# Kernel optimization log

Hardware: AMD Instinct MI355X
Metric: run time of the kernel (lower is better)

The kernel has to match this reference:

```python
import jax, jax.numpy as jnp
import numpy as np

B, S, H, NH = 8, 2048, 256, 4
D = H // NH
EPS = 1e-12


def setup_inputs() -> dict:
    key = jax.random.key(0)
    ks = jax.random.split(key, 8)
    w = lambda k: jax.random.normal(k, (H, H), jnp.float32) * 0.02
    return {
        "input_tensor": jax.random.normal(ks[0], (B, S, H), jnp.float32),
        "attribute_table": jax.random.normal(ks[1], (B, S, 1, H), jnp.float32),
        "position_embedding": jax.random.normal(ks[2], (B, S, H), jnp.float32),
        "attention_mask": jnp.zeros((B, 1, S, S), jnp.float32),
        "Wq": w(ks[3]), "bq": jnp.zeros((H,), jnp.float32),
        "Wk": w(ks[4]), "bk": jnp.zeros((H,), jnp.float32),
        "Wv": w(ks[5]), "bv": jnp.zeros((H,), jnp.float32),
        "Wd": w(ks[6]), "bd": jnp.zeros((H,), jnp.float32),
        "gamma": jnp.ones((H,), jnp.float32),
        "beta": jnp.zeros((H,), jnp.float32),
    }


def _layer_norm(x, g, b):
    mu = jnp.mean(x, axis=-1, keepdims=True)
    var = jnp.mean(jnp.square(x - mu), axis=-1, keepdims=True)
    return (x - mu) * jax.lax.rsqrt(var + EPS) * g + b


def reference(input_tensor, attribute_table, position_embedding, attention_mask,
              Wq, bq, Wk, bk, Wv, bv, Wd, bd, gamma, beta):
    # fusion_type == 'sum': sum attribute tables + item emb + position emb
    mixed = jnp.sum(attribute_table, axis=-2) + input_tensor + position_embedding  # [B,S,H]
    q = (mixed @ Wq + bq).reshape(B, S, NH, D)
    k = (mixed @ Wk + bk).reshape(B, S, NH, D)
    v = (input_tensor @ Wv + bv).reshape(B, S, NH, D)  # value from raw item emb
    scores = jnp.einsum('bqhd,bkhd->bhqk', q, k) / jnp.sqrt(jnp.float32(D))
    scores = scores + attention_mask  # additive mask broadcast over heads
    probs = jax.nn.softmax(scores, axis=-1)  # attn_dropout p=0 (eval)
    ctx = jnp.einsum('bhqk,bkhd->bqhd', probs, v).reshape(B, S, H)
    hidden = ctx @ Wd + bd  # out_dropout p=0 (eval)
    return _layer_norm(hidden + input_tensor, gamma, beta)
```

## Files before the change

kernel.cpp:

```cpp
#include <hip/hip_runtime.h>
#include <hip/hip_bf16.h>
#include <math.h>

#define BB 8
#define SS 2048
#define HH 256
#define NHH 4
#define DD 64
#define MROWS (BB*SS)
#define LOG2E 1.44269504f

typedef unsigned short u16;
typedef unsigned int   u32;
typedef __attribute__((ext_vector_type(8))) short bf16x8;
typedef __attribute__((ext_vector_type(4))) float f32x4;
typedef __attribute__((ext_vector_type(8))) u16   u16x8;
typedef __attribute__((ext_vector_type(4))) u16   u16x4;

__device__ inline u16 f2bf(float f) {
    union { float f; u32 u; } v; v.f = f;
    u32 r = v.u + 0x7fffu + ((v.u >> 16) & 1u);
    return (u16)(r >> 16);
}
__device__ inline u16 f2bf_n(float f) {
    __hip_bfloat16 h = __float2bfloat16(f);
    return *(u16*)&h;
}
__device__ inline float bf2f(u16 h) {
    union { u32 u; float f; } v; v.u = (u32)h << 16; return v.f;
}
__device__ inline float fexp2(float x) {
#if __has_builtin(__builtin_amdgcn_exp2f)
    return __builtin_amdgcn_exp2f(x);
#else
    return __expf(x * 0.6931471806f);
#endif
}
__device__ inline void gload16(const u16* g, u16* l) {
    __builtin_amdgcn_global_load_lds(
        (const __attribute__((address_space(1))) u32*)g,
        (__attribute__((address_space(3))) u32*)l, 16, 0, 0);
}

__global__ __launch_bounds__(256) void fuse_mixed_cast(const float* __restrict__ inp,
    const float* __restrict__ attr, const float* __restrict__ pos,
    u16* __restrict__ mixed, u16* __restrict__ inpb, int n8) {
    int i = blockIdx.x * 256 + threadIdx.x;
    if (i >= n8) return;
    const f32x4* pi = (const f32x4*)(inp  + (size_t)i*8);
    const f32x4* pa = (const f32x4*)(attr + (size_t)i*8);
    const f32x4* pp = (const f32x4*)(pos  + (size_t)i*8);
    u16x8 om, oi;
    #pragma unroll
    for (int h = 0; h < 2; ++h) {
        f32x4 a = pi[h], b = pa[h], c = pp[h];
        #pragma unroll
        for (int j = 0; j < 4; ++j) {
            om[h*4+j] = f2bf(a[j] + b[j] + c[j]);
            oi[h*4+j] = f2bf(a[j]);
        }
    }
    *(u16x8*)(mixed + (size_t)i*8) = om;
    *(u16x8*)(inpb  + (size_t)i*8) = oi;
}

__global__ __launch_bounds__(256) void transpose_w(const float* __restrict__ W0,
    const float* __restrict__ W1, const float* __restrict__ W2,
    const float* __restrict__ W3, u16* __restrict__ Wt) {
    const float* W = blockIdx.y==0 ? W0 : blockIdx.y==1 ? W1 : blockIdx.y==2 ? W2 : W3;
    u16* dst = Wt + (size_t)blockIdx.y*65536;
    int kt = blockIdx.x & 3, nt = blockIdx.x >> 2;
    __shared__ float T[64][65];
    int tid = threadIdx.x;
    int r = tid >> 2, cq = tid & 3;
    const float* src = W + (size_t)(kt*64 + r)*HH + nt*64 + cq*16;
    #pragma unroll
    for (int j = 0; j < 4; ++j) {
        f32x4 v = ((const f32x4*)src)[j];
        T[r][cq*16 + j*4 + 0] = v[0];
        T[r][cq*16 + j*4 + 1] = v[1];
        T[r][cq*16 + j*4 + 2] = v[2];
        T[r][cq*16 + j*4 + 3] = v[3];
    }
    __syncthreads();
    u16x8 o0, o1;
    #pragma unroll
    for (int j = 0; j < 8; ++j) o0[j] = f2bf(T[cq*16 + j][r]);
    #pragma unroll
    for (int j = 0; j < 8; ++j) o1[j] = f2bf(T[cq*16 + 8 + j][r]);
    u16* d = dst + (size_t)(nt*64 + r)*HH + kt*64 + cq*16;
    *(u16x8*)d       = o0;
    *(u16x8*)(d + 8) = o1;
}

template<bool VT>
__global__ __launch_bounds__(256) void gemm_mfma(
    const u16* __restrict__ A0, const u16* __restrict__ A1,
    const u16* __restrict__ Wt, const float* __restrict__ bias0,
    const float* __restrict__ bias1, u16* __restrict__ O0, u16* __restrict__ O1)
{
    __shared__ u16 As[2][128*64];
    __shared__ u16 Ws[2][128*64];
    int tid = threadIdx.x;
    int w = tid >> 6, l = tid & 63;
    int lq = l & 15, g4 = l >> 4;
    int w0 = w >> 1, w1 = w & 1;
    int z = blockIdx.z;
    const u16* A = z ? A1 : A0;
    const u16* Wz = Wt + (size_t)z*65536;
    const float* bias = z ? bias1 : bias0;
    u16* Oz = z ? O1 : O0;
    int bm = blockIdx.x*128, bn = blockIdx.y*128;

    int rr0 = l >> 3;
    int cc0 = (l & 7) ^ (rr0 & 7);
    const u16* agp[4]; const u16* wgp[4];
    #pragma unroll
    for (int q = 0; q < 4; ++q) {
        int rr = (w*4+q)*8 + rr0;
        agp[q] = A  + (size_t)(bm + rr)*HH + cc0*8;
        wgp[q] = Wz + (size_t)(bn + rr)*HH + cc0*8;
    }

    f32x4 acc[4][4];
    #pragma unroll
    for (int i = 0; i < 4; ++i)
        #pragma unroll
        for (int j = 0; j < 4; ++j) acc[i][j] = (f32x4){0.f,0.f,0.f,0.f};

    #define STAGE(buf, k0) { \
        _Pragma("unroll") \
        for (int q = 0; q < 4; ++q) { \
            gload16(agp[q] + (k0), &As[buf][(w*4+q)*512]); \
            gload16(wgp[q] + (k0), &Ws[buf][(w*4+q)*512]); \
        } }

    STAGE(0, 0);
    __syncthreads();
    int cur = 0;
    #pragma unroll
    for (int t = 0; t < 4; ++t) {
        if (t < 3) STAGE(cur^1, (t+1)*64);
        #pragma unroll
        for (int kk = 0; kk < 2; ++kk) {
            bf16x8 af[4], wf[4];
            #pragma unroll
            for (int i = 0; i < 4; ++i) {
                int row = w0*64 + i*16 + lq;
                int cc = (kk*4 + g4) ^ (row & 7);
                af[i] = *(const bf16x8*)&As[cur][row*64 + cc*8];
            }
            #pragma unroll
            for (int j = 0; j < 4; ++j) {
                int row = w1*64 + j*16 + lq;
                int cc = (kk*4 + g4) ^ (row & 7);
                wf[j] = *(const bf16x8*)&Ws[cur][row*64 + cc*8];
            }
            #pragma unroll
            for (int i = 0; i < 4; ++i)
                #pragma unroll
                for (int j = 0; j < 4; ++j) {
                    if (VT)
                        acc[i][j] = __builtin_amdgcn_mfma_f32_16x16x32_bf16(af[i], wf[j], acc[i][j], 0,0,0);
                    else
                        acc[i][j] = __builtin_amdgcn_mfma_f32_16x16x32_bf16(wf[j], af[i], acc[i][j], 0,0,0);
                }
        }
        __syncthreads();
        cur ^= 1;
    }

    if (!VT) {
        #pragma unroll
        for (int i = 0; i < 4; ++i) {
            size_t m = bm + w0*64 + i*16 + lq;
            #pragma unroll
            for (int j = 0; j < 4; ++j) {
                int n = bn + w1*64 + j*16 + g4*4;
                f32x4 bb = *(const f32x4*)&bias[n];
                u16x4 o;
                #pragma unroll
                for (int r = 0; r < 4; ++r) o[r] = f2bf(acc[i][j][r] + bb[r]);
                *(u16x4*)&Oz[m*HH + n] = o;
            }
        }
    } else {
        int b = bm >> 11;
        int sb = bm & 2047;
        #pragma unroll
        for (int i = 0; i < 4; ++i) {
            int s = sb + w0*64 + i*16 + g4*4;
            #pragma unroll
            for (int j = 0; j < 4; ++j) {
                int n = bn + w1*64 + j*16 + lq;
                float bs = bias[n];
                int h = n >> 6, d = n & 63;
                u16x4 o;
                #pragma unroll
                for (int r = 0; r < 4; ++r) o[r] = f2bf(acc[i][j][r] + bs);
                *(u16x4*)&Oz[(((size_t)b*NHH + h)*DD + d)*SS + s] = o;
            }
        }
    }
    #undef STAGE
}

__global__ __launch_bounds__(256) void attn_mfma(
    const u16* __restrict__ Qb, const u16* __restrict__ Kb,
    const u16* __restrict__ Vt, const float* __restrict__ mask,
    u16* __restrict__ O)
{
    __shared__ u16 KT[2][64*64];
    __shared__ u16 VTs[2][64*64];
    __shared__ u16 PT[4][16*64];

    int tid = threadIdx.x;
    int w = tid >> 6, l = tid & 63;
    int lq = l & 15, g = l >> 4;
    int qb = blockIdx.x, h = blockIdx.y, b = blockIdx.z;
    int q = qb*64 + w*16 + lq;

    bf16x8 qf[2];
    {
        const u16* qp = Qb + ((size_t)(b*SS + q))*HH + h*DD + g*8;
        qf[0] = *(const bf16x8*)qp;
        qf[1] = *(const bf16x8*)(qp + 32);
    }

    int srow = tid >> 3;
    int sch  = tid & 7;
    const u16* kgp0 = Kb + ((size_t)(b*SS + srow))*HH + h*DD + sch*8;
    const u16* kgp1 = kgp0 + (size_t)32*HH;
    const u16* vgp0 = Vt + (((size_t)(b*NHH + h))*DD + srow)*SS + sch*8;
    const u16* vgp1 = vgp0 + (size_t)32*SS;
    int sidx0 = srow*64 + ((sch ^ (srow & 7)))*8;
    int sidx1 = sidx0 + 32*64;

    const float* mrow = mask + ((size_t)b*SS + q)*SS + g*4;

    f32x4 ot[4];
    #pragma unroll
    for (int dt = 0; dt < 4; ++dt) ot[dt] = (f32x4){0.f,0.f,0.f,0.f};
    float m = -1e30f, lsum = 0.f;

    u16x8 kr0 = *(const u16x8*)kgp0;
    u16x8 kr1 = *(const u16x8*)kgp1;
    u16x8 vr0 = *(const u16x8*)vgp0;
    u16x8 vr1 = *(const u16x8*)vgp1;
    f32x4 mr[2][4];
    #pragma unroll
    for (int kt = 0; kt < 4; ++kt) mr[0][kt] = *(const f32x4*)(mrow + kt*16);
    *(u16x8*)&KT[0][sidx0]  = kr0;
    *(u16x8*)&KT[0][sidx1]  = kr1;
    *(u16x8*)&VTs[0][sidx0] = vr0;
    *(u16x8*)&VTs[0][sidx1] = vr1;
    __syncthreads();

    #pragma unroll 2
    for (int t = 0; t < SS/64; ++t) {
        int cur = t & 1;
        if (t < SS/64 - 1) {
            kr0 = *(const u16x8*)(kgp0 + (size_t)(t+1)*64*HH);
            kr1 = *(const u16x8*)(kgp1 + (size_t)(t+1)*64*HH);
            vr0 = *(const u16x8*)(vgp0 + (t+1)*64);
            vr1 = *(const u16x8*)(vgp1 + (t+1)*64);
            #pragma unroll
            for (int kt = 0; kt < 4; ++kt)
                mr[cur^1][kt] = *(const f32x4*)(mrow + (t+1)*64 + kt*16);
        }

        f32x4 st[4];
        __builtin_amdgcn_s_setprio(1);
        #pragma unroll
        for (int kt = 0; kt < 4; ++kt) {
            st[kt] = (f32x4){0.f,0.f,0.f,0.f};
            int key = kt*16 + lq;
            #pragma unroll
            for (int df = 0; df < 2; ++df) {
                int c = (4*df + g) ^ (key & 7);
                bf16x8 a = *(const bf16x8*)&KT[cur][key*64 + c*8];
                st[kt] = __builtin_amdgcn_mfma_f32_16x16x32_bf16(a, qf[df], st[kt], 0,0,0);
            }
        }
        __builtin_amdgcn_s_setprio(0);

        float s[4][4];
        #pragma unroll
        for (int kt = 0; kt < 4; ++kt)
            #pragma unroll
            for (int j = 0; j < 4; ++j)
                s[kt][j] = __builtin_fmaf(st[kt][j], 0.125f, mr[cur][kt][j]);

        float cm[4];
        #pragma unroll
        for (int kt = 0; kt < 4; ++kt)
            cm[kt] = fmaxf(fmaxf(s[kt][0], s[kt][1]), fmaxf(s[kt][2], s[kt][3]));
        float tm = fmaxf(fmaxf(cm[0], cm[1]), fmaxf(cm[2], cm[3]));
        tm = fmaxf(tm, __shfl_xor(tm, 16));
        tm = fmaxf(tm, __shfl_xor(tm, 32));

        if (!__all(tm <= m + 8.0f)) {
            float mn = fmaxf(m, tm);
            float sc = fexp2((m - mn) * LOG2E);
            lsum *= sc;
            #pragma unroll
            for (int dt = 0; dt < 4; ++dt) {
                ot[dt][0] *= sc; ot[dt][1] *= sc;
                ot[dt][2] *= sc; ot[dt][3] *= sc;
            }
            m = mn;
        }
        float mnl = m * LOG2E;

        float e[4][4];
        #pragma unroll
        for (int kt = 0; kt < 4; ++kt)
            #pragma unroll
            for (int j = 0; j < 4; ++j)
                e[kt][j] = fexp2(__builtin_fmaf(s[kt][j], LOG2E, -mnl));
        float cs[4];
        #pragma unroll
        for (int kt = 0; kt < 4; ++kt)
            cs[kt] = (e[kt][0] + e[kt][1]) + (e[kt][2] + e[kt][3]);
        float rs = (cs[0] + cs[1]) + (cs[2] + cs[3]);
        rs += __shfl_xor(rs, 16);
        rs += __shfl_xor(rs, 32);
        lsum += rs;

        #pragma unroll
        for (int kt = 0; kt < 4; ++kt) {
            u16x4 pk;
            #pragma unroll
            for (int j = 0; j < 4; ++j) pk[j] = f2bf_n(e[kt][j]);
            int koff = kt*16 + g*4;
            int c = (koff >> 3) ^ (lq & 7);
            int idx = lq*64 + c*8 + (koff & 7);
            *(u16x4*)&PT[w][idx] = pk;
        }

        bf16x8 pb[2];
        #pragma unroll
        for (int kt2 = 0; kt2 < 2; ++kt2) {
            int c = (4*kt2 + g) ^ (lq & 7);
            pb[kt2] = *(const bf16x8*)&PT[w][lq*64 + c*8];
        }
        __builtin_amdgcn_s_setprio(1);
        #pragma unroll
        for (int dt = 0; dt < 4; ++dt) {
            int d = dt*16 + lq;
            #pragma unroll
            for (int kt2 = 0; kt2 < 2; ++kt2) {
                int c = (4*kt2 + g) ^ (d & 7);
                bf16x8 a = *(const bf16x8*)&VTs[cur][d*64 + c*8];
                ot[dt] = __builtin_amdgcn_mfma_f32_16x16x32_bf16(a, pb[kt2], ot[dt], 0,0,0);
            }
        }
        __builtin_amdgcn_s_setprio(0);

        if (t < SS/64 - 1) {
            *(u16x8*)&KT[cur^1][sidx0]  = kr0;
            *(u16x8*)&KT[cur^1][sidx1]  = kr1;
            *(u16x8*)&VTs[cur^1][sidx0] = vr0;
            *(u16x8*)&VTs[cur^1][sidx1] = vr1;
        }
        __syncthreads();
    }

    float inv = 1.0f / lsum;
    #pragma unroll
    for (int dt = 0; dt < 4; ++dt) {
        u16x4 o;
        #pragma unroll
        for (int j = 0; j < 4; ++j) o[j] = f2bf_n(ot[dt][j] * inv);
        *(u16x4*)&O[((size_t)(b*SS + q))*HH + h*DD + dt*16 + g*4] = o;
    }
}

__global__ __launch_bounds__(256) void add_ln(const u16* __restrict__ hidden,
    const u16* __restrict__ inpb, const float* __restrict__ gamma,
    const float* __restrict__ beta, float* __restrict__ out) {
    int row = blockIdx.x;
    int tid = threadIdx.x;
    int lane = tid & 63, wave = tid >> 6;
    __shared__ float red[8];
    float x = bf2f(hidden[(size_t)row*HH + tid]) + bf2f(inpb[(size_t)row*HH + tid]);
    float s = x;
    #pragma unroll
    for (int o = 32; o; o >>= 1) s += __shfl_xor(s, o);
    if (!lane) red[wave] = s;
    __syncthreads();
    float mu = (red[0] + red[1] + red[2] + red[3]) * (1.0f/HH);
    float dx = x - mu;
    float v = dx * dx;
    #pragma unroll
    for (int o = 32; o; o >>= 1) v += __shfl_xor(v, o);
    if (!lane) red[4 + wave] = v;
    __syncthreads();
    float var = (red[4] + red[5] + red[6] + red[7]) * (1.0f/HH);
    out[(size_t)row*HH + tid] = dx * rsqrtf(var + 1e-12f) * gamma[tid] + beta[tid];
}

extern "C" void kernel_launch(void* const* d_in, const int* in_sizes, int n_in,
                              void* d_out, int out_size, void* d_ws, size_t ws_size,
                              hipStream_t stream) {
    const float* inp   = (const float*)d_in[0];
    const float* attr  = (const float*)d_in[1];
    const float* pos   = (const float*)d_in[2];
    const float* mask  = (const float*)d_in[3];
    const float* Wq    = (const float*)d_in[4];
    const float* bq    = (const float*)d_in[5];
    const float* Wk    = (const float*)d_in[6];
    const float* bk    = (const float*)d_in[7];
    const float* Wv    = (const float*)d_in[8];
    const float* bv    = (const float*)d_in[9];
    const float* Wd    = (const float*)d_in[10];
    const float* bd    = (const float*)d_in[11];
    const float* gamma = (const float*)d_in[12];
    const float* beta  = (const float*)d_in[13];
    float* out = (float*)d_out;

    const size_t NEL = (size_t)BB*SS*HH;
    u16* mixed = (u16*)d_ws;
    u16* inpb  = mixed + NEL;
    u16* Qb    = mixed + 2*NEL;
    u16* Kb    = mixed + 3*NEL;
    u16* Vtb   = mixed + 4*NEL;
    u16* ctx   = mixed + 5*NEL;
    u16* hid   = mixed + 6*NEL;
    u16* Wt    = mixed + 7*NEL;

    fuse_mixed_cast<<<(int)(NEL/8/256), 256, 0, stream>>>(inp, attr, pos, mixed, inpb, (int)(NEL/8));
    transpose_w<<<dim3(16,4), 256, 0, stream>>>(Wq, Wk, Wv, Wd, Wt);

    gemm_mfma<false><<<dim3(128,2,2), 256, 0, stream>>>(mixed, mixed, Wt, bq, bk, Qb, Kb);
    gemm_mfma<true ><<<dim3(128,2,1), 256, 0, stream>>>(inpb, inpb, Wt + 2*65536, bv, bv, Vtb, Vtb);

    attn_mfma<<<dim3(SS/64, NHH, BB), 256, 0, stream>>>(Qb, Kb, Vtb, mask, ctx);

    gemm_mfma<false><<<dim3(128,2,1), 256, 0, stream>>>(ctx, ctx, Wt + 3*65536, bd, bd, hid, hid);

    add_ln<<<MROWS, 256, 0, stream>>>(hid, inpb, gamma, beta, out);
}
```

Measured before the change: 163.3 us.

## Switch attention to 32x32 MFMA tiles with register-only P via permlane swap

The attention kernel moves from 16x16x32 to 32x32x16 bf16 MFMA, so each wave handles 32 queries and each block 128 queries, which halves the grid and the K/V LDS loads per query. The probability matrix no longer round-trips through shared memory. It is packed with v_cvt_pk_bf16_f32 and rearranged across lane halves with permlane32_swap straight into the B operand. The mask prefetch moves later in the loop, and launch bounds request 2 blocks per CU. The cost is higher register pressure from the 16-wide accumulators, and the smaller grid (512 blocks) gives less parallelism.

```diff
diff --git a/kernel.cpp b/kernel.cpp
--- a/kernel.cpp
+++ b/kernel.cpp
@@ -12,10 +12,12 @@
 
 typedef unsigned short u16;
 typedef unsigned int   u32;
-typedef __attribute__((ext_vector_type(8))) short bf16x8;
-typedef __attribute__((ext_vector_type(4))) float f32x4;
-typedef __attribute__((ext_vector_type(8))) u16   u16x8;
-typedef __attribute__((ext_vector_type(4))) u16   u16x4;
+typedef __attribute__((ext_vector_type(8)))  short bf16x8;
+typedef __attribute__((ext_vector_type(4)))  float f32x4;
+typedef __attribute__((ext_vector_type(16))) float f32x16;
+typedef __attribute__((ext_vector_type(8)))  u16   u16x8;
+typedef __attribute__((ext_vector_type(4)))  u16   u16x4;
+typedef __attribute__((ext_vector_type(2)))  u32   u32x2;
 
 __device__ inline u16 f2bf(float f) {
     union { float f; u32 u; } v; v.f = f;
@@ -34,6 +36,23 @@
     return __builtin_amdgcn_exp2f(x);
 #else
     return __expf(x * 0.6931471806f);
+#endif
+}
+__device__ inline u32 cvtpk_bf16(float a, float b) {
+    u32 r;
+    asm("v_cvt_pk_bf16_f32 %0, %1, %2" : "=v"(r) : "v"(a), "v"(b));
+    return r;
+}
+__device__ inline u32x2 plswap(u32 a, u32 b, int hi) {
+#if __has_builtin(__builtin_amdgcn_permlane32_swap)
+    return __builtin_amdgcn_permlane32_swap(a, b, false, false);
+#else
+    u32 sa = (u32)__shfl_xor((int)a, 32);
+    u32 sb = (u32)__shfl_xor((int)b, 32);
+    u32x2 r;
+    r.x = hi ? sb : a;
+    r.y = hi ? b : sa;
+    return r;
 #endif
 }
 __device__ inline void gload16(const u16* g, u16* l) {
@@ -205,26 +224,26 @@
     #undef STAGE
 }
 
-__global__ __launch_bounds__(256) void attn_mfma(
+__global__ __launch_bounds__(256, 2) void attn_mfma(
     const u16* __restrict__ Qb, const u16* __restrict__ Kb,
     const u16* __restrict__ Vt, const float* __restrict__ mask,
     u16* __restrict__ O)
 {
     __shared__ u16 KT[2][64*64];
     __shared__ u16 VTs[2][64*64];
-    __shared__ u16 PT[4][16*64];
 
     int tid = threadIdx.x;
     int w = tid >> 6, l = tid & 63;
-    int lq = l & 15, g = l >> 4;
+    int lq = l & 31;
+    int hi = l >> 5;
     int qb = blockIdx.x, h = blockIdx.y, b = blockIdx.z;
-    int q = qb*64 + w*16 + lq;
-
-    bf16x8 qf[2];
+    int q = qb*128 + w*32 + lq;
+
+    bf16x8 qf[4];
     {
-        const u16* qp = Qb + ((size_t)(b*SS + q))*HH + h*DD + g*8;
-        qf[0] = *(const bf16x8*)qp;
-        qf[1] = *(const bf16x8*)(qp + 32);
+        const u16* qp = Qb + ((size_t)(b*SS + q))*HH + h*DD + hi*8;
+        #pragma unroll
+        for (int kf = 0; kf < 4; ++kf) qf[kf] = *(const bf16x8*)(qp + kf*16);
     }
 
     int srow = tid >> 3;
@@ -236,20 +255,25 @@
     int sidx0 = srow*64 + ((sch ^ (srow & 7)))*8;
     int sidx1 = sidx0 + 32*64;
 
-    const float* mrow = mask + ((size_t)b*SS + q)*SS + g*4;
-
-    f32x4 ot[4];
-    #pragma unroll
-    for (int dt = 0; dt < 4; ++dt) ot[dt] = (f32x4){0.f,0.f,0.f,0.f};
+    const float* mrow = mask + ((size_t)b*SS + q)*SS + hi*4;
+
+    f32x16 ot[2];
+    #pragma unroll
+    for (int dt = 0; dt < 2; ++dt)
+        #pragma unroll
+        for (int r = 0; r < 16; ++r) ot[dt][r] = 0.f;
     float m = -1e30f, lsum = 0.f;
 
     u16x8 kr0 = *(const u16x8*)kgp0;
     u16x8 kr1 = *(const u16x8*)kgp1;
     u16x8 vr0 = *(const u16x8*)vgp0;
     u16x8 vr1 = *(const u16x8*)vgp1;
-    f32x4 mr[2][4];
-    #pragma unroll
-    for (int kt = 0; kt < 4; ++kt) mr[0][kt] = *(const f32x4*)(mrow + kt*16);
+    f32x4 mq[2][4];
+    #pragma unroll
+    for (int kt = 0; kt < 2; ++kt)
+        #pragma unroll
+        for (int g = 0; g < 4; ++g)
+            mq[kt][g] = *(const f32x4*)(mrow + kt*32 + g*8);
     *(u16x8*)&KT[0][sidx0]  = kr0;
     *(u16x8*)&KT[0][sidx1]  = kr1;
     *(u16x8*)&VTs[0][sidx0] = vr0;
@@ -264,39 +288,40 @@
             kr1 = *(const u16x8*)(kgp1 + (size_t)(t+1)*64*HH);
             vr0 = *(const u16x8*)(vgp0 + (t+1)*64);
             vr1 = *(const u16x8*)(vgp1 + (t+1)*64);
-            #pragma unroll
-            for (int kt = 0; kt < 4; ++kt)
-                mr[cur^1][kt] = *(const f32x4*)(mrow + (t+1)*64 + kt*16);
-        }
-
-        f32x4 st[4];
+        }
+
+        f32x16 st[2];
         __builtin_amdgcn_s_setprio(1);
         #pragma unroll
-        for (int kt = 0; kt < 4; ++kt) {
-            st[kt] = (f32x4){0.f,0.f,0.f,0.f};
-            int key = kt*16 + lq;
-            #pragma unroll
-            for (int df = 0; df < 2; ++df) {
-                int c = (4*df + g) ^ (key & 7);
-                bf16x8 a = *(const bf16x8*)&KT[cur][key*64 + c*8];
-                st[kt] = __builtin_amdgcn_mfma_f32_16x16x32_bf16(a, qf[df], st[kt], 0,0,0);
+        for (int kt = 0; kt < 2; ++kt) {
+            #pragma unroll
+            for (int r = 0; r < 16; ++r) st[kt][r] = 0.f;
+            int row = kt*32 + lq;
+            #pragma unroll
+            for (int kf = 0; kf < 4; ++kf) {
+                int c = (kf*2 + hi) ^ (lq & 7);
+                bf16x8 a = *(const bf16x8*)&KT[cur][row*64 + c*8];
+                st[kt] = __builtin_amdgcn_mfma_f32_32x32x16_bf16(a, qf[kf], st[kt], 0,0,0);
             }
         }
         __builtin_amdgcn_s_setprio(0);
 
-        float s[4][4];
-        #pragma unroll
-        for (int kt = 0; kt < 4; ++kt)
-            #pragma unroll
-            for (int j = 0; j < 4; ++j)
-                s[kt][j] = __builtin_fmaf(st[kt][j], 0.125f, mr[cur][kt][j]);
-
-        float cm[4];
-        #pragma unroll
-        for (int kt = 0; kt < 4; ++kt)
-            cm[kt] = fmaxf(fmaxf(s[kt][0], s[kt][1]), fmaxf(s[kt][2], s[kt][3]));
-        float tm = fmaxf(fmaxf(cm[0], cm[1]), fmaxf(cm[2], cm[3]));
-        tm = fmaxf(tm, __shfl_xor(tm, 16));
+        float s[2][16];
+        #pragma unroll
+        for (int kt = 0; kt < 2; ++kt)
+            #pragma unroll
+            for (int r = 0; r < 16; ++r)
+                s[kt][r] = __builtin_fmaf(st[kt][r], 0.125f, mq[kt][r>>2][r&3]);
+
+        float mx[8];
+        #pragma unroll
+        for (int i = 0; i < 8; ++i) {
+            float a = fmaxf(s[i>>2][(i&3)*4+0], s[i>>2][(i&3)*4+1]);
+            float c = fmaxf(s[i>>2][(i&3)*4+2], s[i>>2][(i&3)*4+3]);
+            mx[i] = fmaxf(a, c);
+        }
+        float tm = fmaxf(fmaxf(fmaxf(mx[0],mx[1]), fmaxf(mx[2],mx[3])),
+                         fmaxf(fmaxf(mx[4],mx[5]), fmaxf(mx[6],mx[7])));
         tm = fmaxf(tm, __shfl_xor(tm, 32));
 
         if (!__all(tm <= m + 8.0f)) {
@@ -304,55 +329,62 @@
             float sc = fexp2((m - mn) * LOG2E);
             lsum *= sc;
             #pragma unroll
-            for (int dt = 0; dt < 4; ++dt) {
-                ot[dt][0] *= sc; ot[dt][1] *= sc;
-                ot[dt][2] *= sc; ot[dt][3] *= sc;
-            }
+            for (int dt = 0; dt < 2; ++dt)
+                #pragma unroll
+                for (int r = 0; r < 16; ++r) ot[dt][r] *= sc;
             m = mn;
         }
         float mnl = m * LOG2E;
 
-        float e[4][4];
-        #pragma unroll
-        for (int kt = 0; kt < 4; ++kt)
-            #pragma unroll
-            for (int j = 0; j < 4; ++j)
-                e[kt][j] = fexp2(__builtin_fmaf(s[kt][j], LOG2E, -mnl));
-        float cs[4];
-        #pragma unroll
-        for (int kt = 0; kt < 4; ++kt)
-            cs[kt] = (e[kt][0] + e[kt][1]) + (e[kt][2] + e[kt][3]);
-        float rs = (cs[0] + cs[1]) + (cs[2] + cs[3]);
-        rs += __shfl_xor(rs, 16);
+        #pragma unroll
+        for (int kt = 0; kt < 2; ++kt)
+            #pragma unroll
+            for (int r = 0; r < 16; ++r)
+                s[kt][r] = fexp2(__builtin_fmaf(s[kt][r], LOG2E, -mnl));
+        float sm[8];
+        #pragma unroll
+        for (int i = 0; i < 8; ++i)
+            sm[i] = (s[i>>2][(i&3)*4+0] + s[i>>2][(i&3)*4+1])
+                  + (s[i>>2][(i&3)*4+2] + s[i>>2][(i&3)*4+3]);
+        float rs = ((sm[0]+sm[1]) + (sm[2]+sm[3])) + ((sm[4]+sm[5]) + (sm[6]+sm[7]));
         rs += __shfl_xor(rs, 32);
         lsum += rs;
 
-        #pragma unroll
-        for (int kt = 0; kt < 4; ++kt) {
-            u16x4 pk;
-            #pragma unroll
-            for (int j = 0; j < 4; ++j) pk[j] = f2bf_n(e[kt][j]);
-            int koff = kt*16 + g*4;
-            int c = (koff >> 3) ^ (lq & 7);
-            int idx = lq*64 + c*8 + (koff & 7);
-            *(u16x4*)&PT[w][idx] = pk;
-        }
-
-        bf16x8 pb[2];
-        #pragma unroll
-        for (int kt2 = 0; kt2 < 2; ++kt2) {
-            int c = (4*kt2 + g) ^ (lq & 7);
-            pb[kt2] = *(const bf16x8*)&PT[w][lq*64 + c*8];
-        }
+        if (t < SS/64 - 1) {
+            #pragma unroll
+            for (int kt = 0; kt < 2; ++kt)
+                #pragma unroll
+                for (int g = 0; g < 4; ++g)
+                    mq[kt][g] = *(const f32x4*)(mrow + (t+1)*64 + kt*32 + g*8);
+        }
+
+        bf16x8 pb[4];
+        #pragma unroll
+        for (int kt = 0; kt < 2; ++kt) {
+            u32 wd[8];
+            #pragma unroll
+            for (int i = 0; i < 8; ++i)
+                wd[i] = cvtpk_bf16(s[kt][2*i], s[kt][2*i+1]);
+            u32x2 r02 = plswap(wd[0], wd[2], hi);
+            u32x2 r13 = plswap(wd[1], wd[3], hi);
+            u32x2 r46 = plswap(wd[4], wd[6], hi);
+            u32x2 r57 = plswap(wd[5], wd[7], hi);
+            union { u32 u[4]; bf16x8 v; } p0, p1;
+            p0.u[0] = r02.x; p0.u[1] = r13.x; p0.u[2] = r02.y; p0.u[3] = r13.y;
+            p1.u[0] = r46.x; p1.u[1] = r57.x; p1.u[2] = r46.y; p1.u[3] = r57.y;
+            pb[kt*2+0] = p0.v;
+            pb[kt*2+1] = p1.v;
+        }
+
         __builtin_amdgcn_s_setprio(1);
         #pragma unroll
-        for (int dt = 0; dt < 4; ++dt) {
-            int d = dt*16 + lq;
-            #pragma unroll
-            for (int kt2 = 0; kt2 < 2; ++kt2) {
-                int c = (4*kt2 + g) ^ (d & 7);
-                bf16x8 a = *(const bf16x8*)&VTs[cur][d*64 + c*8];
-                ot[dt] = __builtin_amdgcn_mfma_f32_16x16x32_bf16(a, pb[kt2], ot[dt], 0,0,0);
+        for (int dt = 0; dt < 2; ++dt) {
+            int row = dt*32 + lq;
+            #pragma unroll
+            for (int kt2 = 0; kt2 < 4; ++kt2) {
+                int c = (kt2*2 + hi) ^ (lq & 7);
+                bf16x8 a = *(const bf16x8*)&VTs[cur][row*64 + c*8];
+                ot[dt] = __builtin_amdgcn_mfma_f32_32x32x16_bf16(a, pb[kt2], ot[dt], 0,0,0);
             }
         }
         __builtin_amdgcn_s_setprio(0);
@@ -367,12 +399,16 @@
     }
 
     float inv = 1.0f / lsum;
-    #pragma unroll
-    for (int dt = 0; dt < 4; ++dt) {
-        u16x4 o;
-        #pragma unroll
-        for (int j = 0; j < 4; ++j) o[j] = f2bf_n(ot[dt][j] * inv);
-        *(u16x4*)&O[((size_t)(b*SS + q))*HH + h*DD + dt*16 + g*4] = o;
+    u16* orow = O + ((size_t)(b*SS + q))*HH + h*DD + hi*4;
+    #pragma unroll
+    for (int dt = 0; dt < 2; ++dt) {
+        #pragma unroll
+        for (int r4 = 0; r4 < 4; ++r4) {
+            u16x4 o;
+            #pragma unroll
+            for (int j = 0; j < 4; ++j) o[j] = f2bf_n(ot[dt][r4*4+j] * inv);
+            *(u16x4*)(orow + dt*32 + r4*8) = o;
+        }
     }
 }
 
@@ -435,7 +471,7 @@
     gemm_mfma<false><<<dim3(128,2,2), 256, 0, stream>>>(mixed, mixed, Wt, bq, bk, Qb, Kb);
     gemm_mfma<true ><<<dim3(128,2,1), 256, 0, stream>>>(inpb, inpb, Wt + 2*65536, bv, bv, Vtb, Vtb);
 
-    attn_mfma<<<dim3(SS/64, NHH, BB), 256, 0, stream>>>(Qb, Kb, Vtb, mask, ctx);
+    attn_mfma<<<dim3(SS/128, NHH, BB), 256, 0, stream>>>(Qb, Kb, Vtb, mask, ctx);
 
     gemm_mfma<false><<<dim3(128,2,1), 256, 0, stream>>>(ctx, ctx, Wt + 3*65536, bd, bd, hid, hid);
 
```

After: 140.1 us. 14.2% less time.
